# Performance work log

Hardware: AMD Instinct MI355X
Metric: run time of the kernel (lower is better)

Reference implementation:

```python
import jax, jax.numpy as jnp
import numpy as np

D_MODEL = 1024
N_HEADS = 16
D_K = D_MODEL // N_HEADS
SCALE = 1.0 / np.sqrt(D_K).astype(np.float32)
NEG = -1000000000.0


def setup_inputs() -> dict:
    key = jax.random.key(0)
    ks = jax.random.split(key, 5)
    B, S = 2, 2048
    query = jax.random.normal(ks[0], (B, S, D_MODEL), dtype=jnp.float32)
    k_in = jax.random.normal(ks[1], (B, S, D_MODEL), dtype=jnp.float32)
    v_in = jax.random.normal(ks[2], (B, S, D_MODEL), dtype=jnp.float32)
    # causal mask, broadcast over batch and heads; 0 entries get -1e9
    mask = jnp.tril(jnp.ones((S, S), dtype=jnp.int32))[None, None, :, :]
    w_qkv = jax.random.normal(ks[3], (D_MODEL, 3 * D_MODEL), dtype=jnp.float32) * (1.0 / np.sqrt(D_MODEL))
    w_o = jax.random.normal(ks[4], (D_MODEL, D_MODEL), dtype=jnp.float32) * (1.0 / np.sqrt(D_MODEL))
    return {"query": query, "key": k_in, "value": v_in, "mask": mask, "w_qkv": w_qkv, "w_o": w_o}


def reference(query, key, value, mask, w_qkv, w_o):
    # NOTE: original module ignores `key`/`value`; q,k,v all come from `query`.
    B, S, _ = query.shape
    qkv = query @ w_qkv                       # [B,S,3D]
    q, k, v = jnp.split(qkv, 3, axis=-1)
    def heads(x):
        return x.reshape(B, S, N_HEADS, D_K).transpose(0, 2, 1, 3)  # [B,H,S,dk]
    Q, K, V = heads(q), heads(k), heads(v)
    scores = jnp.einsum('bhqd,bhkd->bhqk', Q, K) * SCALE            # [B,H,S,S]
    scores = jnp.where(mask == 0, NEG, scores)
    attn = jax.nn.softmax(scores, axis=-1)
    # Dropout(0.1) treated as eval-mode identity for a deterministic reference.
    context = jnp.einsum('bhqk,bhkd->bhqd', attn, V)                # [B,H,S,dk]
    context = context.transpose(0, 2, 1, 3).reshape(B, S, D_MODEL)
    return context @ w_o
```

## Files before the change

kernel.cpp:

```cpp
#include <hip/hip_runtime.h>
#include <stdint.h>


typedef __attribute__((ext_vector_type(8))) short bf16x8;
typedef __attribute__((ext_vector_type(4))) float f32x4;

#define LOG2E 1.44269504088896340736f
#define QSCALE (0.125f * LOG2E)

__device__ __forceinline__ unsigned short f2b(float f) {
  union { float f; unsigned int i; } x; x.f = f;
  unsigned int i = x.i;
  return (unsigned short)((i + 0x7FFFu + ((i >> 16) & 1u)) >> 16);
}

__device__ __forceinline__ void async16(const void* g, void* l) {
  __builtin_amdgcn_global_load_lds(
      (__attribute__((address_space(1))) void*)g,
      (__attribute__((address_space(3))) void*)l, 16, 0, 0);
}

__device__ __forceinline__ f32x4 mfma16(bf16x8 a, bf16x8 b, f32x4 c) {
  return __builtin_amdgcn_mfma_f32_16x16x32_bf16(a, b, c, 0, 0, 0);
}

__device__ __forceinline__ unsigned int fbits(float f) {
  union { float f; unsigned int i; } x; x.f = f;
  return x.i;
}

__global__ __launch_bounds__(256) void prep(
    const float* __restrict__ X, const float* __restrict__ Wqkv,
    const float* __restrict__ Wo, unsigned short* __restrict__ Xb,
    unsigned short* __restrict__ WqkvT, unsigned short* __restrict__ WoT) {
  __shared__ __align__(16) unsigned short Lt[64 * 64];
  const int bx = blockIdx.x;
  const int t = threadIdx.x;
  if (bx < 2048) {
    const size_t i = ((size_t)bx * 256 + t) * 8;
    float4 a = *(const float4*)(X + i);
    float4 b = *(const float4*)(X + i + 4);
    unsigned short e[8];
    e[0] = f2b(a.x); e[1] = f2b(a.y); e[2] = f2b(a.z); e[3] = f2b(a.w);
    e[4] = f2b(b.x); e[5] = f2b(b.y); e[6] = f2b(b.z); e[7] = f2b(b.w);
    *(uint4*)(Xb + i) = *(const uint4*)e;
    return;
  }
  const bool is_qkv = (bx < 2816);
  const int bid = is_qkv ? bx - 2048 : bx - 2816;
  const float* src = is_qkv ? Wqkv : Wo;
  unsigned short* dst = is_qkv ? WqkvT : WoT;
  const int Ccols = is_qkv ? 3072 : 1024;
  const int r0 = (bid & 15) * 64, c0 = (bid >> 4) * 64;
  const float s = (is_qkv && c0 < 1024) ? QSCALE : 1.0f;
#pragma unroll
  for (int it = 0; it < 4; ++it) {
    int c = it * 256 + t;
    int sr = c >> 4, co = (c & 15) * 4;
    float4 v = *(const float4*)(src + (size_t)(r0 + sr) * Ccols + c0 + co);
    Lt[(co + 0) * 64 + sr] = f2b(v.x * s);
    Lt[(co + 1) * 64 + sr] = f2b(v.y * s);
    Lt[(co + 2) * 64 + sr] = f2b(v.z * s);
    Lt[(co + 3) * 64 + sr] = f2b(v.w * s);
  }
  __syncthreads();
#pragma unroll
  for (int it = 0; it < 2; ++it) {
    int c = it * 256 + t;
    int dr = c >> 3, so = (c & 7) * 8;
    *(uint4*)(dst + (size_t)(c0 + dr) * 1024 + r0 + so) =
        *(const uint4*)(Lt + dr * 64 + so);
  }
}

__global__ __launch_bounds__(256) void gemm_qkv(
    const unsigned short* __restrict__ A, const unsigned short* __restrict__ Bt,
    unsigned short* __restrict__ C, unsigned short* __restrict__ Vt) {
  constexpr int K = 1024, N = 3072;
  __shared__ __align__(16) unsigned short Sm[16896];
  unsigned short* As = Sm;
  unsigned short* Bs = Sm + 8192;
  unsigned short* Lt = Sm;

  const int t = threadIdx.x;
  const int w = t >> 6, l = t & 63;
  const int m0 = blockIdx.y * 128, n0 = blockIdx.x * 128;
  const int wm = (w >> 1) * 64, wn = (w & 1) * 64;
  const int lrow = l & 15, lq = l >> 4;

  f32x4 acc[4][4] = {};

  for (int k0 = 0; k0 < K; k0 += 64) {
    __syncthreads();
#pragma unroll
    for (int r = 0; r < 4; ++r) {
      const int c = r * 256 + t;
      const int row = c >> 3;
      const int so = ((c & 7) ^ (row & 7)) * 8;
      async16(A + (size_t)(m0 + row) * K + k0 + so,
              As + (size_t)(r * 256 + t) * 8);
      async16(Bt + (size_t)(n0 + row) * K + k0 + so,
              Bs + (size_t)(r * 256 + t) * 8);
    }
    asm volatile("s_waitcnt vmcnt(0)" ::: "memory");
    __syncthreads();

#pragma unroll
    for (int kh = 0; kh < 2; ++kh) {
      bf16x8 af[4], bf[4];
      const int phys = ((kh * 4 + lq) ^ (lrow & 7)) * 8;
#pragma unroll
      for (int i = 0; i < 4; ++i)
        af[i] = *(const bf16x8*)(As + (wm + i * 16 + lrow) * 64 + phys);
#pragma unroll
      for (int j = 0; j < 4; ++j)
        bf[j] = *(const bf16x8*)(Bs + (wn + j * 16 + lrow) * 64 + phys);
#pragma unroll
      for (int i = 0; i < 4; ++i)
#pragma unroll
        for (int j = 0; j < 4; ++j)
          acc[i][j] = mfma16(af[i], bf[j], acc[i][j]);
    }
  }

  if (n0 < 2048) {
#pragma unroll
    for (int i = 0; i < 4; ++i)
#pragma unroll
      for (int j = 0; j < 4; ++j)
#pragma unroll
        for (int r = 0; r < 4; ++r) {
          int gr = m0 + wm + i * 16 + lq * 4 + r;
          int gc = n0 + wn + j * 16 + lrow;
          C[(size_t)gr * N + gc] = f2b(acc[i][j][r]);
        }
  } else {
    __syncthreads();
#pragma unroll
    for (int i = 0; i < 4; ++i)
#pragma unroll
      for (int j = 0; j < 4; ++j) {
        int col_loc = wn + j * 16 + lrow;
        int row_loc = wm + i * 16 + lq * 4;
        uint2 pk;
        pk.x = (unsigned int)f2b(acc[i][j][0]) |
               ((unsigned int)f2b(acc[i][j][1]) << 16);
        pk.y = (unsigned int)f2b(acc[i][j][2]) |
               ((unsigned int)f2b(acc[i][j][3]) << 16);
        *(uint2*)(Lt + col_loc * 132 + row_loc) = pk;
      }
    __syncthreads();
    const int b = m0 >> 11, s0 = m0 & 2047;
    const int vb0 = n0 - 2048;
#pragma unroll
    for (int rnd = 0; rnd < 8; ++rnd) {
      int vrow = rnd * 16 + (t >> 4);
      int sloc = (t & 15) * 8;
      int vcol = vb0 + vrow;
      int bh = b * 16 + (vcol >> 6);
      int d = vcol & 63;
      *(uint4*)(Vt + ((size_t)bh * 64 + d) * 2048 + s0 + sloc) =
          *(const uint4*)(Lt + vrow * 132 + sloc);
    }
  }
}

__global__ __launch_bounds__(256) void gemm_o(
    const unsigned short* __restrict__ A, const unsigned short* __restrict__ Bt,
    float* __restrict__ C, int M, int N, int K) {
  __shared__ __align__(16) unsigned short As[64 * 64];
  __shared__ __align__(16) unsigned short Bs[128 * 64];
  const int t = threadIdx.x;
  const int w = t >> 6, l = t & 63;
  const int m0 = blockIdx.y * 64, n0 = blockIdx.x * 128;
  const int wm = (w & 1) * 32, wn = (w >> 1) * 64;
  const int lrow = l & 15, lq = l >> 4;

  f32x4 acc[2][4] = {};

  for (int k0 = 0; k0 < K; k0 += 64) {
    __syncthreads();
#pragma unroll
    for (int r = 0; r < 2; ++r) {
      const int c = r * 256 + t;
      const int row = c >> 3;
      const int so = ((c & 7) ^ (row & 7)) * 8;
      async16(A + (size_t)(m0 + row) * K + k0 + so,
              As + (size_t)(r * 256 + t) * 8);
    }
#pragma unroll
    for (int r = 0; r < 4; ++r) {
      const int c = r * 256 + t;
      const int row = c >> 3;
      const int so = ((c & 7) ^ (row & 7)) * 8;
      async16(Bt + (size_t)(n0 + row) * K + k0 + so,
              Bs + (size_t)(r * 256 + t) * 8);
    }
    asm volatile("s_waitcnt vmcnt(0)" ::: "memory");
    __syncthreads();

#pragma unroll
    for (int kh = 0; kh < 2; ++kh) {
      bf16x8 af[2], bf[4];
      const int phys = ((kh * 4 + lq) ^ (lrow & 7)) * 8;
#pragma unroll
      for (int i = 0; i < 2; ++i)
        af[i] = *(const bf16x8*)(As + (wm + i * 16 + lrow) * 64 + phys);
#pragma unroll
      for (int j = 0; j < 4; ++j)
        bf[j] = *(const bf16x8*)(Bs + (wn + j * 16 + lrow) * 64 + phys);
#pragma unroll
      for (int i = 0; i < 2; ++i)
#pragma unroll
        for (int j = 0; j < 4; ++j)
          acc[i][j] = mfma16(af[i], bf[j], acc[i][j]);
    }
  }

#pragma unroll
  for (int i = 0; i < 2; ++i)
#pragma unroll
    for (int j = 0; j < 4; ++j)
#pragma unroll
      for (int r = 0; r < 4; ++r) {
        int gr = m0 + wm + i * 16 + lq * 4 + r;
        int gc = n0 + wn + j * 16 + lrow;
        C[(size_t)gr * N + gc] = acc[i][j][r];
      }
}

__global__ __launch_bounds__(512, 4) void attn_fwd(
    const unsigned short* __restrict__ qkv,
    const unsigned short* __restrict__ Vt,
    unsigned short* __restrict__ ctx) {
  __shared__ __align__(16) unsigned short Ks[2][64 * 64];
  __shared__ __align__(16) unsigned short Vs[2][64 * 64];
  __shared__ __align__(16) unsigned short Ps[8][16 * 72];

  const int ti = blockIdx.x;
  const int bh = blockIdx.y;
  const int b = bh >> 4, h = bh & 15;
  const int t = threadIdx.x;
  const int g = t >> 8;
  const int tl = t & 255;
  const int w = tl >> 6;
  const int gw = t >> 6;
  const int l = t & 63;
  const int lm = l & 15, lq = l >> 4;
  const int sw = lm & 7;
  const int c0 = (lq ^ sw) * 8;
  const int c1 = ((lq + 4) ^ sw) * 8;

  const int qt0[2] = {ti * 64, (31 - ti) * 64};
  const int ktmax = 31 - ti;
  const int nsup = (ktmax >> 1) + 1;

  const unsigned short* Qp = qkv + (size_t)(b * 2048) * 3072 + h * 64;
  const unsigned short* Kp = qkv + (size_t)(b * 2048) * 3072 + 1024 + h * 64;
  const unsigned short* Vb = Vt + (size_t)bh * 64 * 2048;

  bf16x8 qf[2][2];
#pragma unroll
  for (int qt = 0; qt < 2; ++qt) {
    const int qrow = qt0[qt] + w * 16 + lm;
    qf[qt][0] = *(const bf16x8*)(Qp + (size_t)qrow * 3072 + lq * 8);
    qf[qt][1] = *(const bf16x8*)(Qp + (size_t)qrow * 3072 + 32 + lq * 8);
  }

  f32x4 oacc[2][4] = {};
  float lsum[2] = {0.f, 0.f};

  for (int jj = 0; jj < nsup; ++jj) {
    const int kt = 2 * jj + g;
    const bool have = (kt <= ktmax);
    __syncthreads();
    if (have) {
      const int kk0 = kt * 64;
#pragma unroll
      for (int r = 0; r < 2; ++r) {
        int cl = r * 256 + tl;
        int row = cl >> 3, cp = cl & 7;
        int so = ((cp ^ (row & 7)) * 8);
        async16(Kp + (size_t)(kk0 + row) * 3072 + so,
                Ks[g] + (size_t)(r * 256 + w * 64) * 8);
        async16(Vb + (size_t)row * 2048 + kk0 + so,
                Vs[g] + (size_t)(r * 256 + w * 64) * 8);
      }
    }
    asm volatile("s_waitcnt vmcnt(0)" ::: "memory");
    __syncthreads();
    if (!have) continue;

    const unsigned short* Kc = Ks[g];
    const unsigned short* Vc = Vs[g];

    bf16x8 vf[8];
#pragma unroll
    for (int nt = 0; nt < 4; ++nt) {
      const unsigned short* vr = Vc + (nt * 16 + lm) * 64;
      vf[nt] = *(const bf16x8*)(vr + c0);
      vf[4 + nt] = *(const bf16x8*)(vr + c1);
    }

#pragma unroll
    for (int qt = 0; qt < 2; ++qt) {
      if (qt == 0 && kt > ti) continue;
      f32x4 sacc[4] = {};
#pragma unroll
      for (int mt = 0; mt < 4; ++mt) {
        const unsigned short* kr = Kc + (mt * 16 + lm) * 64;
        bf16x8 bk0 = *(const bf16x8*)(kr + c0);
        bf16x8 bk1 = *(const bf16x8*)(kr + c1);
        sacc[mt] = mfma16(bk0, qf[qt][0], sacc[mt]);
        sacc[mt] = mfma16(bk1, qf[qt][1], sacc[mt]);
      }

      const bool diag = (kt == ((qt == 0) ? ti : ktmax));
      const int qloc = w * 16 + lm;
#pragma unroll
      for (int mt = 0; mt < 4; ++mt) {
        float p0 = __builtin_amdgcn_exp2f(sacc[mt][0]);
        float p1 = __builtin_amdgcn_exp2f(sacc[mt][1]);
        float p2 = __builtin_amdgcn_exp2f(sacc[mt][2]);
        float p3 = __builtin_amdgcn_exp2f(sacc[mt][3]);
        if (diag) {
          const int kvb = mt * 16 + lq * 4;
          if (kvb + 0 > qloc) p0 = 0.f;
          if (kvb + 1 > qloc) p1 = 0.f;
          if (kvb + 2 > qloc) p2 = 0.f;
          if (kvb + 3 > qloc) p3 = 0.f;
        }
        lsum[qt] += (p0 + p1) + (p2 + p3);
        uint2 pk;
        pk.x = (fbits(p1) & 0xFFFF0000u) | (fbits(p0) >> 16);
        pk.y = (fbits(p3) & 0xFFFF0000u) | (fbits(p2) >> 16);
        *(uint2*)(&Ps[gw][lm * 72 + mt * 16 + lq * 4]) = pk;
      }
      asm volatile("s_waitcnt lgkmcnt(0)" ::: "memory");

#pragma unroll
      for (int ks = 0; ks < 2; ++ks) {
        bf16x8 pa = *(const bf16x8*)(&Ps[gw][lm * 72 + ks * 32 + lq * 8]);
#pragma unroll
        for (int nt = 0; nt < 4; ++nt)
          oacc[qt][nt] = mfma16(pa, vf[ks * 4 + nt], oacc[qt][nt]);
      }
    }
  }

#pragma unroll
  for (int qt = 0; qt < 2; ++qt) {
    lsum[qt] += __shfl_xor(lsum[qt], 16, 64);
    lsum[qt] += __shfl_xor(lsum[qt], 32, 64);
  }

  __syncthreads();
  float* fbuf[2] = {(float*)Ks, (float*)Vs};
  float* lbuf = (float*)Ps;
  if (g == 1) {
#pragma unroll
    for (int qt = 0; qt < 2; ++qt) {
#pragma unroll
      for (int nt = 0; nt < 4; ++nt)
#pragma unroll
        for (int r = 0; r < 4; ++r)
          fbuf[qt][(w * 16 + lq * 4 + r) * 64 + nt * 16 + lm] = oacc[qt][nt][r];
      if (l < 16) lbuf[qt * 64 + w * 16 + lm] = lsum[qt];
    }
  }
  __syncthreads();
  if (g == 0) {
#pragma unroll
    for (int qt = 0; qt < 2; ++qt) {
      const float ltot = lsum[qt] + lbuf[qt * 64 + w * 16 + lm];
      float rinv[4];
#pragma unroll
      for (int r = 0; r < 4; ++r)
        rinv[r] = 1.f / __shfl(ltot, lq * 4 + r, 64);
#pragma unroll
      for (int nt = 0; nt < 4; ++nt)
#pragma unroll
        for (int r = 0; r < 4; ++r) {
          float v = oacc[qt][nt][r] +
                    fbuf[qt][(w * 16 + lq * 4 + r) * 64 + nt * 16 + lm];
          size_t tok = (size_t)b * 2048 + qt0[qt] + w * 16 + lq * 4 + r;
          ctx[tok * 1024 + h * 64 + nt * 16 + lm] = f2b(v * rinv[r]);
        }
    }
  }
}

extern "C" void kernel_launch(void* const* d_in, const int* in_sizes, int n_in,
                              void* d_out, int out_size, void* d_ws,
                              size_t ws_size, hipStream_t stream) {
  const float* query = (const float*)d_in[0];
  const float* w_qkv = (const float*)d_in[4];
  const float* w_o = (const float*)d_in[5];
  float* out = (float*)d_out;

  unsigned short* ws = (unsigned short*)d_ws;
  unsigned short* wqkvT = ws;
  unsigned short* woT = wqkvT + (size_t)3072 * 1024;
  unsigned short* Xb = woT + (size_t)1024 * 1024;
  unsigned short* qkv = Xb + (size_t)4096 * 1024;
  unsigned short* Vt = qkv + (size_t)4096 * 3072;
  unsigned short* ctx = Xb;

  prep<<<dim3(3072), 256, 0, stream>>>(query, w_qkv, w_o, Xb, wqkvT, woT);
  gemm_qkv<<<dim3(24, 32), 256, 0, stream>>>(Xb, wqkvT, qkv, Vt);
  attn_fwd<<<dim3(16, 32), 512, 0, stream>>>(qkv, Vt, ctx);
  gemm_o<<<dim3(8, 64), 256, 0, stream>>>(ctx, woT, out, 4096, 1024, 1024);
}
```

Measured before the change: 202.1 us.

## Register-prefetch next K/V tile, remap block indices, raise MFMA wave priority

Replaces the synchronous global_load_lds K/V loads, which waited on vmcnt(0) before each tile, with a register double-buffer. The next tile's K/V is loaded into registers while the current tile is computed, then stored to LDS at the top of the next iteration. Block indices are also remapped so that blocks sharing a batch-head or query tile are spread differently across CUs. s_setprio is raised around the MFMA sections. The register prefetch increases VGPR pressure, which under launch_bounds(512,4) could cause spills or lower occupancy.

```diff
diff --git a/kernel.cpp b/kernel.cpp
--- a/kernel.cpp
+++ b/kernel.cpp
@@ -237,8 +237,9 @@
   __shared__ __align__(16) unsigned short Vs[2][64 * 64];
   __shared__ __align__(16) unsigned short Ps[8][16 * 72];
 
-  const int ti = blockIdx.x;
-  const int bh = blockIdx.y;
+  const int idx = (blockIdx.x >> 3) + 2 * blockIdx.y;
+  const int bh = (blockIdx.x & 7) * 4 + (idx >> 4);
+  const int ti = idx & 15;
   const int b = bh >> 4, h = bh & 15;
   const int t = threadIdx.x;
   const int g = t >> 8;
@@ -270,25 +271,44 @@
   f32x4 oacc[2][4] = {};
   float lsum[2] = {0.f, 0.f};
 
+  const int row0 = tl >> 3, cp = tl & 7;
+  const int row1 = row0 + 32;
+  const int so0 = (cp ^ (row0 & 7)) * 8;
+  const int so1 = (cp ^ (row1 & 7)) * 8;
+  const unsigned short* kg0 = Kp + (size_t)(g * 64 + row0) * 3072 + so0;
+  const unsigned short* kg1 = Kp + (size_t)(g * 64 + row1) * 3072 + so1;
+  const unsigned short* vg0 = Vb + (size_t)row0 * 2048 + g * 64 + so0;
+  const unsigned short* vg1 = Vb + (size_t)row1 * 2048 + g * 64 + so1;
+  unsigned short* kd0 = Ks[g] + (size_t)tl * 8;
+  unsigned short* kd1 = Ks[g] + (size_t)(256 + tl) * 8;
+  unsigned short* vd0 = Vs[g] + (size_t)tl * 8;
+  unsigned short* vd1 = Vs[g] + (size_t)(256 + tl) * 8;
+
+  uint4 kr0 = *(const uint4*)kg0;
+  uint4 kr1 = *(const uint4*)kg1;
+  uint4 vr0 = *(const uint4*)vg0;
+  uint4 vr1 = *(const uint4*)vg1;
+
   for (int jj = 0; jj < nsup; ++jj) {
     const int kt = 2 * jj + g;
     const bool have = (kt <= ktmax);
     __syncthreads();
     if (have) {
-      const int kk0 = kt * 64;
-#pragma unroll
-      for (int r = 0; r < 2; ++r) {
-        int cl = r * 256 + tl;
-        int row = cl >> 3, cp = cl & 7;
-        int so = ((cp ^ (row & 7)) * 8);
-        async16(Kp + (size_t)(kk0 + row) * 3072 + so,
-                Ks[g] + (size_t)(r * 256 + w * 64) * 8);
-        async16(Vb + (size_t)row * 2048 + kk0 + so,
-                Vs[g] + (size_t)(r * 256 + w * 64) * 8);
-      }
-    }
-    asm volatile("s_waitcnt vmcnt(0)" ::: "memory");
-    __syncthreads();
+      *(uint4*)kd0 = kr0;
+      *(uint4*)kd1 = kr1;
+      *(uint4*)vd0 = vr0;
+      *(uint4*)vd1 = vr1;
+    }
+    __syncthreads();
+
+    if (kt + 2 <= ktmax) {
+      kg0 += 128 * 3072; kg1 += 128 * 3072;
+      vg0 += 128; vg1 += 128;
+      kr0 = *(const uint4*)kg0;
+      kr1 = *(const uint4*)kg1;
+      vr0 = *(const uint4*)vg0;
+      vr1 = *(const uint4*)vg1;
+    }
     if (!have) continue;
 
     const unsigned short* Kc = Ks[g];
@@ -306,6 +326,7 @@
     for (int qt = 0; qt < 2; ++qt) {
       if (qt == 0 && kt > ti) continue;
       f32x4 sacc[4] = {};
+      __builtin_amdgcn_s_setprio(1);
 #pragma unroll
       for (int mt = 0; mt < 4; ++mt) {
         const unsigned short* kr = Kc + (mt * 16 + lm) * 64;
@@ -314,6 +335,7 @@
         sacc[mt] = mfma16(bk0, qf[qt][0], sacc[mt]);
         sacc[mt] = mfma16(bk1, qf[qt][1], sacc[mt]);
       }
+      __builtin_amdgcn_s_setprio(0);
 
       const bool diag = (kt == ((qt == 0) ? ti : ktmax));
       const int qloc = w * 16 + lm;
@@ -338,6 +360,7 @@
       }
       asm volatile("s_waitcnt lgkmcnt(0)" ::: "memory");
 
+      __builtin_amdgcn_s_setprio(1);
 #pragma unroll
       for (int ks = 0; ks < 2; ++ks) {
         bf16x8 pa = *(const bf16x8*)(&Ps[gw][lm * 72 + ks * 32 + lq * 8]);
@@ -345,6 +368,7 @@
         for (int nt = 0; nt < 4; ++nt)
           oacc[qt][nt] = mfma16(pa, vf[ks * 4 + nt], oacc[qt][nt]);
       }
+      __builtin_amdgcn_s_setprio(0);
     }
   }
 
```

New measurement: 220.3 us. +9.0%, slower.
